# Performance work log

Measured on AMD Instinct MI355X. Metric: run time of the kernel, lower is better.

## Reference

```python
import jax, jax.numpy as jnp
import numpy as np

VOCAB = 50000
NUM_TAGS = 12
EMBED_DIM = 300
HIDDEN_DIM = 300
B, S = 64, 256
START_IDX = NUM_TAGS - 2
STOP_IDX = NUM_TAGS - 1
NEG = -10000.0


def setup_inputs() -> dict:
    key = jax.random.key(0)
    ks = jax.random.split(key, 12)
    # tokens in [1, VOCAB) so mask = (sentences != 0) is all ones (full-length, sorted)
    sentences = jax.random.randint(ks[0], (B, S), 1, VOCAB)
    tags = jax.random.randint(ks[1], (B, S), 0, NUM_TAGS)
    embed_table = jax.random.normal(ks[2], (VOCAB, EMBED_DIM), jnp.float32)
    k = 1.0 / np.sqrt(HIDDEN_DIM)
    u = lambda kk, shp: jax.random.uniform(kk, shp, jnp.float32, -k, k)
    # PyTorch LSTM gate order: i, f, g, o. b = b_ih + b_hh fused.
    W_ih_f = u(ks[3], (4 * HIDDEN_DIM, EMBED_DIM))
    W_hh_f = u(ks[4], (4 * HIDDEN_DIM, HIDDEN_DIM))
    b_f = u(ks[5], (4 * HIDDEN_DIM,))
    W_ih_b = u(ks[6], (4 * HIDDEN_DIM, EMBED_DIM))
    W_hh_b = u(ks[7], (4 * HIDDEN_DIM, HIDDEN_DIM))
    b_b = u(ks[8], (4 * HIDDEN_DIM,))
    kl = 1.0 / np.sqrt(2 * HIDDEN_DIM)
    W_lin = jax.random.uniform(ks[9], (NUM_TAGS, 2 * HIDDEN_DIM), jnp.float32, -kl, kl)
    b_lin = jax.random.uniform(ks[10], (NUM_TAGS,), jnp.float32, -kl, kl)
    transitions = jax.random.uniform(ks[11], (NUM_TAGS, NUM_TAGS), jnp.float32)
    transitions = transitions.at[START_IDX, :].set(NEG)
    transitions = transitions.at[:, STOP_IDX].set(NEG)
    return dict(sentences=sentences, tags=tags, embed_table=embed_table,
                W_ih_f=W_ih_f, W_hh_f=W_hh_f, b_f=b_f,
                W_ih_b=W_ih_b, W_hh_b=W_hh_b, b_b=b_b,
                W_lin=W_lin, b_lin=b_lin, transitions=transitions)


def _lstm_scan(x_seq, W_ih, W_hh, b):
    # x_seq: (S, B, E) -> (S, B, H)
    H = W_hh.shape[1]
    Bb = x_seq.shape[1]

    def step(carry, x_t):
        h, c = carry
        g = x_t @ W_ih.T + h @ W_hh.T + b
        i, f, gg, o = jnp.split(g, 4, axis=-1)
        c = jax.nn.sigmoid(f) * c + jax.nn.sigmoid(i) * jnp.tanh(gg)
        h = jax.nn.sigmoid(o) * jnp.tanh(c)
        return (h, c), h

    init = (jnp.zeros((Bb, H), x_seq.dtype), jnp.zeros((Bb, H), x_seq.dtype))
    _, hs = jax.lax.scan(step, init, x_seq)
    return hs


def reference(sentences, tags, embed_table, W_ih_f, W_hh_f, b_f,
              W_ih_b, W_hh_b, b_b, W_lin, b_lin, transitions):
    # Embedding, time-major layout (S, B, E)
    x = embed_table[sentences].transpose(1, 0, 2)
    h_f = _lstm_scan(x, W_ih_f, W_hh_f, b_f)
    h_b = jnp.flip(_lstm_scan(jnp.flip(x, 0), W_ih_b, W_hh_b, b_b), 0)
    lstm_out = jnp.concatenate([h_f, h_b], axis=-1)          # (S, B, 2H)
    emit = lstm_out @ W_lin.T + b_lin                         # (S, B, K)
    emit_bsk = emit.transpose(1, 0, 2)                        # (B, S, K)

    # Gold path score (mask is all ones for full-length sequences)
    tok_score = jnp.take_along_axis(emit_bsk, tags[..., None], axis=2).squeeze(2)
    trans_score = transitions[tags[:, :-1], tags[:, 1:]]
    total_score = tok_score.sum(axis=1) + trans_score.sum(axis=1)

    # CRF partition function: forward algorithm over time
    def crf_step(d, e_t):
        # d: (B, K) prev log-alpha; e_t: (B, K) emissions at step t
        # log_sum[b, j, k] = d[b, j] + trans[j, k] + e_t[b, k]
        d_new = jax.nn.logsumexp(d[:, :, None] + transitions[None] + e_t[:, None, :], axis=1)
        return d_new, None

    d0 = emit[0]                                              # (B, K)
    d_final, _ = jax.lax.scan(crf_step, d0, emit[1:])
    log_z = jax.nn.logsumexp(d_final, axis=1)                 # (B,)

    loss = log_z - total_score                                # -log-likelihood per example
    return loss
```

## Files before the change

### kernel.cpp

```cpp
#include <hip/hip_runtime.h>
#include <hip/hip_bf16.h>

static constexpr int BATCH = 64;
static constexpr int SEQ   = 256;
static constexpr int ED    = 300;
static constexpr int HD    = 300;
static constexpr int HPAD  = 320;
static constexpr int GPAD  = 1280;
static constexpr int NTAG  = 12;
static constexpr int NWG_DIR = 10;
static constexpr int NH      = 32;

static constexpr size_t O_GIN  = 0;
static constexpr size_t SZ_GIN = (size_t)2*SEQ*BATCH*GPAD*2;
static constexpr size_t O_H    = O_GIN + SZ_GIN;
static constexpr size_t SZ_H   = (size_t)2*SEQ*NWG_DIR*BATCH*NH*2;
static constexpr size_t O_WHH  = O_H + SZ_H;
static constexpr size_t SZ_WHH = (size_t)2*GPAD*HPAD*2;
static constexpr size_t O_WIH  = O_WHH + SZ_WHH;
static constexpr size_t SZ_WIH = (size_t)2*GPAD*HPAD*2;
static constexpr size_t O_BIAS = O_WIH + SZ_WIH;
static constexpr size_t SZ_BIAS= (size_t)2*GPAD*4;
static constexpr size_t O_EMIT = O_BIAS + SZ_BIAS;
static constexpr size_t SZ_EMIT= (size_t)SEQ*BATCH*NTAG*4;
static constexpr size_t O_CTR  = O_EMIT + SZ_EMIT;

typedef __bf16 bf16x8 __attribute__((ext_vector_type(8)));
typedef float  f32x4  __attribute__((ext_vector_type(4)));
typedef unsigned short u16x8 __attribute__((ext_vector_type(8)));
typedef unsigned short u16;

__device__ __forceinline__ float bu(u16 u){ union{unsigned i; float f;} x; x.i = ((unsigned)u)<<16; return x.f; }
__device__ __forceinline__ u16 fb(float f){ union{float f; unsigned i;} x; x.f = f; unsigned r = x.i + 0x7FFFu + ((x.i>>16)&1u); return (u16)(r>>16); }
__device__ __forceinline__ float sigf(float x){ return 1.0f/(1.0f + __expf(-x)); }
__device__ __forceinline__ float tanh_(float x){ return 2.0f*sigf(2.0f*x) - 1.0f; }
__device__ __forceinline__ f32x4 mfma16(bf16x8 a, bf16x8 b, f32x4 c){
  return __builtin_amdgcn_mfma_f32_16x16x32_bf16(a, b, c, 0, 0, 0);
}
__device__ __forceinline__ int swz4(int r){ return ((r + (r>>2)) & 3); }

__global__ __launch_bounds__(256) void k0_pack(
    const float* whf, const float* whb, const float* wif, const float* wib,
    const float* bfv, const float* bbv,
    u16* wpkhh, u16* wpkih, float* biasPk, int* ctr)
{
  int idx = blockIdx.x*256 + threadIdx.x;
  int mat = idx / (2*GPAD*HPAD);
  int rem = idx % (2*GPAD*HPAD);
  int dd  = rem / (GPAD*HPAD);
  int rr  = rem % (GPAD*HPAD);
  int R   = rr / HPAD, kk = rr % HPAD;
  int jj  = R >> 2, gate = R & 3;
  float v = 0.f;
  if (jj < HD && kk < HD){
    const float* src = mat ? (dd ? wib : wif) : (dd ? whb : whf);
    v = src[(size_t)(gate*HD + jj)*ED + kk];
  }
  (mat ? wpkih : wpkhh)[rem] = fb(v);
  if (idx < 2*GPAD){
    int d2 = idx / GPAD, R2 = idx % GPAD;
    int j2 = R2 >> 2, g2 = R2 & 3;
    biasPk[idx] = (j2 < HD) ? (d2 ? bbv : bfv)[g2*HD + j2] : 0.f;
  }
  if (idx < 2) ctr[idx*64] = 0;
}

__global__ __launch_bounds__(256) void k1_gin(
    const int* sent, const float* embed, const u16* wpkih,
    const float* biasPk, u16* gin)
{
  int blk = blockIdx.x;
  int mb = blk / 40, nb = blk % 40;
  int tid = threadIdx.x, lane = tid & 63, w = tid >> 6;

  __shared__ int srow[64];
  __shared__ u16 sA[64*32];
  __shared__ u16 sB[64*32];

  if (tid < 64) srow[tid] = sent[(size_t)tid*SEQ + mb];
  __syncthreads();

  f32x4 acc[4] = {f32x4{0,0,0,0},f32x4{0,0,0,0},f32x4{0,0,0,0},f32x4{0,0,0,0}};
  int r = tid >> 2, cc = tid & 3;
  int col = lane & 15, hi = lane >> 4;

  for (int k0 = 0; k0 < 10; k0++){
    {
      int kbase = k0*32 + cc*8;
      const float* erow = embed + (size_t)srow[r]*ED;
      float v[8];
      if (kbase + 8 <= ED){
        float4 p0 = *(const float4*)(erow + kbase);
        float4 p1 = *(const float4*)(erow + kbase + 4);
        v[0]=p0.x; v[1]=p0.y; v[2]=p0.z; v[3]=p0.w;
        v[4]=p1.x; v[5]=p1.y; v[6]=p1.z; v[7]=p1.w;
      } else {
        #pragma unroll
        for (int e = 0; e < 8; e++) v[e] = (kbase + e < ED) ? erow[kbase + e] : 0.f;
      }
      u16x8 pk;
      #pragma unroll
      for (int e = 0; e < 8; e++) pk[e] = fb(v[e]);
      *(u16x8*)&sA[r*32 + ((cc ^ swz4(r))*8)] = pk;
      int n = nb*64 + r;
      u16x8 bv = *(const u16x8*)(wpkih + (size_t)n*HPAD + k0*32 + cc*8);
      *(u16x8*)&sB[r*32 + ((cc ^ swz4(r))*8)] = bv;
    }
    __syncthreads();
    {
      int ar = w*16 + col;
      bf16x8 a = *(const bf16x8*)&sA[ar*32 + ((hi ^ swz4(ar))*8)];
      #pragma unroll
      for (int nt = 0; nt < 4; nt++){
        int br = nt*16 + col;
        bf16x8 b = *(const bf16x8*)&sB[br*32 + ((hi ^ swz4(br))*8)];
        acc[nt] = mfma16(a, b, acc[nt]);
      }
    }
    __syncthreads();
  }
  #pragma unroll
  for (int nt = 0; nt < 4; nt++){
    int n_g = nb*64 + nt*16 + col;
    int d = n_g / GPAD, R = n_g % GPAD;
    float bias = biasPk[n_g];
    #pragma unroll
    for (int reg = 0; reg < 4; reg++){
      int b = w*16 + hi*4 + reg;
      float val = acc[nt][reg] + bias;
      gin[(((size_t)d*SEQ + mb)*BATCH + b)*GPAD + R] = fb(val);
    }
  }
}

__global__ __launch_bounds__(256,1) void k2_lstm(
    const u16* wpkhh, const u16* gin, u16* hbuf, int* ctr)
{
  const int tid = threadIdx.x, lane = tid & 63, wid = tid >> 6;
  const int d = blockIdx.x / NWG_DIR, sl = blockIdx.x % NWG_DIR;
  const int mi = wid >> 1, ni = wid & 1;
  const int col = lane & 15, hi = lane >> 4;
  const int gb = tid >> 2, jq = tid & 3;

  __shared__ __align__(16) char smem[40960];
  u16*   sH = (u16*)smem;
  float* sG = (float*)smem;

  bf16x8 Bf[10][4];
  #pragma unroll
  for (int k = 0; k < 10; k++)
    #pragma unroll
    for (int nt = 0; nt < 4; nt++){
      size_t off = ((size_t)d*GPAD + sl*128 + ni*64 + nt*16 + col)*HPAD + k*32 + hi*8;
      Bf[k][nt] = *(const bf16x8*)(wpkhh + off);
    }

  float cst[8];
  #pragma unroll
  for (int q = 0; q < 8; q++) cst[q] = 0.f;

  int* myctr = ctr + d*64;

  for (int rstep = 0; rstep < SEQ; rstep++){
    int t_store = d ? (SEQ-1-rstep) : rstep;

    u16x8 gv[4];
    {
      const u16* gq = gin + (((size_t)d*SEQ + t_store)*BATCH + gb)*GPAD + sl*128 + jq*32;
      #pragma unroll
      for (int m = 0; m < 4; m++) gv[m] = *(const u16x8*)(gq + m*8);
    }

    if (rstep > 0){
      if (tid == 0){
        while (__hip_atomic_load(myctr, __ATOMIC_RELAXED, __HIP_MEMORY_SCOPE_AGENT)
               < NWG_DIR*rstep)
          __builtin_amdgcn_s_sleep(1);
      }
      __syncthreads();
      __builtin_amdgcn_fence(__ATOMIC_ACQUIRE, "agent");

      int t_prev = d ? (t_store+1) : (rstep-1);
      const u16* hsrc = hbuf + (size_t)(d*SEQ + t_prev)*NWG_DIR*BATCH*NH;
      #pragma unroll
      for (int q = 0; q < 10; q++){
        int f = q*256 + tid;
        int b = (f >> 2) & 63;
        int cch = ((f >> 8) << 2) + (f & 3);
        u16x8 v = *(const u16x8*)(hsrc + (size_t)f*8);
        *(u16x8*)&sH[b*320 + ((cch ^ (b&7))*8)] = v;
      }
      __syncthreads();
      f32x4 acc[2][4];
      #pragma unroll
      for (int mt = 0; mt < 2; mt++)
        #pragma unroll
        for (int nt = 0; nt < 4; nt++) acc[mt][nt] = f32x4{0,0,0,0};
      #pragma unroll
      for (int k = 0; k < 10; k++){
        int c = k*4 + hi;
        int r0 = mi*32 + col, r1 = r0 + 16;
        bf16x8 a0 = *(const bf16x8*)&sH[r0*320 + ((c ^ (r0&7))*8)];
        bf16x8 a1 = *(const bf16x8*)&sH[r1*320 + ((c ^ (r1&7))*8)];
        #pragma unroll
        for (int nt = 0; nt < 4; nt++){
          acc[0][nt] = mfma16(a0, Bf[k][nt], acc[0][nt]);
          acc[1][nt] = mfma16(a1, Bf[k][nt], acc[1][nt]);
        }
      }
      __syncthreads();
      #pragma unroll
      for (int mt = 0; mt < 2; mt++)
        #pragma unroll
        for (int nt = 0; nt < 4; nt++){
          int nl = ni*64 + nt*16 + col;
          int bb = mi*32 + mt*16 + hi*4;
          #pragma unroll
          for (int g = 0; g < 4; g++) sG[(bb+g)*132 + nl] = acc[mt][nt][g];
        }
      __syncthreads();
    }

    u16x8 hout;
    #pragma unroll
    for (int ji = 0; ji < 8; ji++){
      float i_ = bu(gv[(ji>>1)][ (ji&1)*4 + 0 ]);
      float f_ = bu(gv[(ji>>1)][ (ji&1)*4 + 1 ]);
      float g_ = bu(gv[(ji>>1)][ (ji&1)*4 + 2 ]);
      float o_ = bu(gv[(ji>>1)][ (ji&1)*4 + 3 ]);
      if (rstep > 0){
        f32x4 r = *(const f32x4*)&sG[gb*132 + (jq*8 + ji)*4];
        i_ += r[0]; f_ += r[1]; g_ += r[2]; o_ += r[3];
      }
      float cn = sigf(f_)*cst[ji] + sigf(i_)*tanh_(g_);
      cst[ji] = cn;
      hout[ji] = (u16)fb(sigf(o_)*tanh_(cn));
    }
    u16* hdst = hbuf + ((size_t)(d*SEQ + t_store)*NWG_DIR + sl)*BATCH*NH + gb*NH + jq*8;
    *(u16x8*)hdst = hout;
    __syncthreads();
    if (tid == 0)
      __hip_atomic_fetch_add(myctr, 1, __ATOMIC_RELEASE, __HIP_MEMORY_SCOPE_AGENT);
  }
}

__global__ __launch_bounds__(256) void k3_emit(
    const u16* hbuf, const float* wlin, const float* blin, float* emit)
{
  int blk = blockIdx.x;
  int t = blk >> 1, b0 = (blk & 1)*32;
  int tid = threadIdx.x;

  __shared__ u16 sh[32*600];
  __shared__ u16 swl[NTAG*600];
  __shared__ float sbl[NTAG];

  for (int p = tid; p < NTAG*600; p += 256) swl[p] = fb(wlin[p]);
  if (tid < NTAG) sbl[tid] = blin[tid];
  for (int p = tid; p < 32*600; p += 256){
    int b = p / 600, c = p % 600;
    int dd = (c < HD) ? 0 : 1;
    int c2 = (c < HD) ? c : (c - HD);
    int sl = c2 >> 5, j = c2 & 31;
    u16 v = hbuf[((size_t)(dd*SEQ + t)*NWG_DIR + sl)*BATCH*NH + (b0 + b)*NH + j];
    sh[p] = v;
  }
  __syncthreads();

  for (int p = tid; p < 32*NTAG; p += 256){
    int b = p & 31, k = p >> 5;
    const u16x8* ha = (const u16x8*)&sh[b*600];
    const u16x8* wa = (const u16x8*)&swl[k*600];
    float s = 0.f;
    #pragma unroll 5
    for (int c = 0; c < 75; c++){
      u16x8 hv = ha[c], wv = wa[c];
      #pragma unroll
      for (int e = 0; e < 8; e++) s += bu(hv[e])*bu(wv[e]);
    }
    emit[((size_t)t*BATCH + b0 + b)*NTAG + k] = s + sbl[k];
  }
}

__global__ __launch_bounds__(256) void k4_crf(
    const float* emit, const int* tags, const float* trans, float* out)
{
  int b0 = blockIdx.x*16;
  int tid = threadIdx.x;
  __shared__ float sT[NTAG*NTAG];
  __shared__ float sd[2][16][NTAG];

  if (tid < NTAG*NTAG) sT[tid] = trans[tid];
  int b = tid / NTAG, k = tid % NTAG;
  bool act = tid < 16*NTAG;
  if (act) sd[0][b][k] = emit[((size_t)0*BATCH + b0 + b)*NTAG + k];
  __syncthreads();

  int cur = 0;
  for (int t = 1; t < SEQ; t++){
    if (act){
      float m = -1e30f;
      #pragma unroll
      for (int j = 0; j < NTAG; j++) m = fmaxf(m, sd[cur][b][j] + sT[j*NTAG + k]);
      float ssum = 0.f;
      #pragma unroll
      for (int j = 0; j < NTAG; j++) ssum += __expf(sd[cur][b][j] + sT[j*NTAG + k] - m);
      sd[cur^1][b][k] = m + __logf(ssum) + emit[((size_t)t*BATCH + b0 + b)*NTAG + k];
    }
    __syncthreads();
    cur ^= 1;
  }

  if (tid < 16){
    int bb = b0 + tid;
    const int* tg = tags + (size_t)bb*SEQ;
    float sc = 0.f; int prev = tg[0];
    sc += emit[((size_t)0*BATCH + bb)*NTAG + prev];
    for (int t = 1; t < SEQ; t++){
      int c2 = tg[t];
      sc += emit[((size_t)t*BATCH + bb)*NTAG + c2] + sT[prev*NTAG + c2];
      prev = c2;
    }
    float m = -1e30f;
    for (int k2 = 0; k2 < NTAG; k2++) m = fmaxf(m, sd[cur][tid][k2]);
    float ssum = 0.f;
    for (int k2 = 0; k2 < NTAG; k2++) ssum += __expf(sd[cur][tid][k2] - m);
    out[bb] = m + __logf(ssum) - sc;
  }
}

extern "C" void kernel_launch(void* const* d_in, const int* in_sizes, int n_in,
                              void* d_out, int out_size, void* d_ws, size_t ws_size,
                              hipStream_t stream)
{
  const int*   sent  = (const int*)  d_in[0];
  const int*   tags  = (const int*)  d_in[1];
  const float* embed = (const float*)d_in[2];
  const float* wif   = (const float*)d_in[3];
  const float* whf   = (const float*)d_in[4];
  const float* bfv   = (const float*)d_in[5];
  const float* wib   = (const float*)d_in[6];
  const float* whb   = (const float*)d_in[7];
  const float* bbv   = (const float*)d_in[8];
  const float* wlin  = (const float*)d_in[9];
  const float* blin  = (const float*)d_in[10];
  const float* trans = (const float*)d_in[11];

  char* ws = (char*)d_ws;
  u16*   gin    = (u16*)  (ws + O_GIN);
  u16*   hbuf   = (u16*)  (ws + O_H);
  u16*   wpkhh  = (u16*)  (ws + O_WHH);
  u16*   wpkih  = (u16*)  (ws + O_WIH);
  float* biasPk = (float*)(ws + O_BIAS);
  float* emit   = (float*)(ws + O_EMIT);
  int*   ctr    = (int*)  (ws + O_CTR);

  k0_pack<<<6400, 256, 0, stream>>>(whf, whb, wif, wib, bfv, bbv,
                                    wpkhh, wpkih, biasPk, ctr);
  k1_gin<<<256*40, 256, 0, stream>>>(sent, embed, wpkih, biasPk, gin);
  k2_lstm<<<2*NWG_DIR, 256, 0, stream>>>(wpkhh, gin, hbuf, ctr);
  k3_emit<<<SEQ*2, 256, 0, stream>>>(hbuf, wlin, blin, emit);
  k4_crf<<<4, 256, 0, stream>>>(emit, tags, trans, (float*)d_out);
}
```

Measured before the change: 2.170 ms.

## Replace shared atomic step counter with per-workgroup flags in LSTM recurrence

The inter-workgroup barrier in the persistent LSTM kernel no longer has every workgroup increment one shared counter. Each workgroup now publishes its own step flag, and the first NWG_DIR threads of each workgroup poll all peer flags in parallel. This is meant to remove contention from the serialized atomic adds and shorten the per-step barrier latency. The hidden-state writes now use relaxed agent-scope atomic stores, and the sG row stride is padded from 132 to 133 to reduce LDS bank conflicts. The flags array is larger and must fit within the existing counter region of the workspace.

After: 2.290 ms. +5.6%, slower.

```diff
diff --git a/kernel.cpp b/kernel.cpp
--- a/kernel.cpp
+++ b/kernel.cpp
@@ -42,7 +42,7 @@
 __global__ __launch_bounds__(256) void k0_pack(
     const float* whf, const float* whb, const float* wif, const float* wib,
     const float* bfv, const float* bbv,
-    u16* wpkhh, u16* wpkih, float* biasPk, int* ctr)
+    u16* wpkhh, u16* wpkih, float* biasPk, int* flags)
 {
   int idx = blockIdx.x*256 + threadIdx.x;
   int mat = idx / (2*GPAD*HPAD);
@@ -62,7 +62,7 @@
     int j2 = R2 >> 2, g2 = R2 & 3;
     biasPk[idx] = (j2 < HD) ? (d2 ? bbv : bfv)[g2*HD + j2] : 0.f;
   }
-  if (idx < 2) ctr[idx*64] = 0;
+  if (idx < 2*NWG_DIR*16) flags[idx] = 0;
 }
 
 __global__ __launch_bounds__(256) void k1_gin(
@@ -134,7 +134,7 @@
 }
 
 __global__ __launch_bounds__(256,1) void k2_lstm(
-    const u16* wpkhh, const u16* gin, u16* hbuf, int* ctr)
+    const u16* wpkhh, const u16* gin, u16* hbuf, int* flags)
 {
   const int tid = threadIdx.x, lane = tid & 63, wid = tid >> 6;
   const int d = blockIdx.x / NWG_DIR, sl = blockIdx.x % NWG_DIR;
@@ -159,7 +159,7 @@
   #pragma unroll
   for (int q = 0; q < 8; q++) cst[q] = 0.f;
 
-  int* myctr = ctr + d*64;
+  int* myflag = flags + (d*NWG_DIR + sl)*16;
 
   for (int rstep = 0; rstep < SEQ; rstep++){
     int t_store = d ? (SEQ-1-rstep) : rstep;
@@ -172,9 +172,9 @@
     }
 
     if (rstep > 0){
-      if (tid == 0){
-        while (__hip_atomic_load(myctr, __ATOMIC_RELAXED, __HIP_MEMORY_SCOPE_AGENT)
-               < NWG_DIR*rstep)
+      if (tid < NWG_DIR){
+        const int* fp = flags + (d*NWG_DIR + tid)*16;
+        while (__hip_atomic_load(fp, __ATOMIC_RELAXED, __HIP_MEMORY_SCOPE_AGENT) < rstep)
           __builtin_amdgcn_s_sleep(1);
       }
       __syncthreads();
@@ -216,7 +216,7 @@
           int nl = ni*64 + nt*16 + col;
           int bb = mi*32 + mt*16 + hi*4;
           #pragma unroll
-          for (int g = 0; g < 4; g++) sG[(bb+g)*132 + nl] = acc[mt][nt][g];
+          for (int g = 0; g < 4; g++) sG[(bb+g)*133 + nl] = acc[mt][nt][g];
         }
       __syncthreads();
     }
@@ -229,18 +229,24 @@
       float g_ = bu(gv[(ji>>1)][ (ji&1)*4 + 2 ]);
       float o_ = bu(gv[(ji>>1)][ (ji&1)*4 + 3 ]);
       if (rstep > 0){
-        f32x4 r = *(const f32x4*)&sG[gb*132 + (jq*8 + ji)*4];
+        f32x4 r = *(const f32x4*)&sG[gb*133 + (jq*8 + ji)*4];
         i_ += r[0]; f_ += r[1]; g_ += r[2]; o_ += r[3];
       }
       float cn = sigf(f_)*cst[ji] + sigf(i_)*tanh_(g_);
       cst[ji] = cn;
       hout[ji] = (u16)fb(sigf(o_)*tanh_(cn));
     }
-    u16* hdst = hbuf + ((size_t)(d*SEQ + t_store)*NWG_DIR + sl)*BATCH*NH + gb*NH + jq*8;
-    *(u16x8*)hdst = hout;
+    {
+      u16* hdst = hbuf + ((size_t)(d*SEQ + t_store)*NWG_DIR + sl)*BATCH*NH + gb*NH + jq*8;
+      union { u16x8 v; unsigned w[4]; } hu; hu.v = hout;
+      unsigned* hd = (unsigned*)hdst;
+      #pragma unroll
+      for (int m = 0; m < 4; m++)
+        __hip_atomic_store(hd + m, hu.w[m], __ATOMIC_RELAXED, __HIP_MEMORY_SCOPE_AGENT);
+    }
     __syncthreads();
     if (tid == 0)
-      __hip_atomic_fetch_add(myctr, 1, __ATOMIC_RELEASE, __HIP_MEMORY_SCOPE_AGENT);
+      __hip_atomic_store(myflag, rstep + 1, __ATOMIC_RELEASE, __HIP_MEMORY_SCOPE_AGENT);
   }
 }
 
@@ -353,12 +359,12 @@
   u16*   wpkih  = (u16*)  (ws + O_WIH);
   float* biasPk = (float*)(ws + O_BIAS);
   float* emit   = (float*)(ws + O_EMIT);
-  int*   ctr    = (int*)  (ws + O_CTR);
+  int*   flags  = (int*)  (ws + O_CTR);
 
   k0_pack<<<6400, 256, 0, stream>>>(whf, whb, wif, wib, bfv, bbv,
-                                    wpkhh, wpkih, biasPk, ctr);
+                                    wpkhh, wpkih, biasPk, flags);
   k1_gin<<<256*40, 256, 0, stream>>>(sent, embed, wpkih, biasPk, gin);
-  k2_lstm<<<2*NWG_DIR, 256, 0, stream>>>(wpkhh, gin, hbuf, ctr);
+  k2_lstm<<<2*NWG_DIR, 256, 0, stream>>>(wpkhh, gin, hbuf, flags);
   k3_emit<<<SEQ*2, 256, 0, stream>>>(hbuf, wlin, blin, emit);
   k4_crf<<<4, 256, 0, stream>>>(emit, tags, trans, (float*)d_out);
 }
```
